# Kernel tuning notes

Measured on AMD Instinct MI355X. Metric: run time of the kernel, lower is better.

Reference implementation:

```python
import jax, jax.numpy as jnp
import numpy as np

N, C, T, V = 32, 64, 256, 25
IC, NS = 16, 3  # inter_channels = C // 4, num_subset = 3
EPS = 1e-5


def _bn(x, g, b, m, v):
    # inference-mode BatchNorm2d over channel dim of [N, C, T, V]
    scale = g / jnp.sqrt(v + EPS)
    return (x - m[:, None, None]) * scale[:, None, None] + b[:, None, None]


def _conv1x1(x, w, b):
    # 1x1 Conv2d on [N, C, T, V]; w: [O, C], b: [O]
    return jnp.einsum('nctv,oc->notv', x, w) + b[None, :, None, None]


def setup_inputs() -> dict:
    key = jax.random.key(0)
    ks = iter(jax.random.split(key, 40))
    def nrm(shape, s=0.05):
        return jax.random.normal(next(ks), shape, jnp.float32) * s
    inp = {}
    inp['feature'] = jax.random.normal(next(ks), (N, C, T, V), jnp.float32)
    inp['hidden'] = jax.random.normal(next(ks), (N, C, T, V), jnp.float32)
    inp['A'] = jax.random.uniform(next(ks), (NS, V, V), jnp.float32) * 0.1
    inp['PA'] = jnp.full((NS, V, V), 1e-6, jnp.float32)
    inp['conv_a_w'] = nrm((NS, IC, C)); inp['conv_a_b'] = nrm((NS, IC))
    inp['conv_b_w'] = nrm((NS, IC, C)); inp['conv_b_b'] = nrm((NS, IC))
    inp['conv_d_w'] = nrm((NS, C, C));  inp['conv_d_b'] = nrm((NS, C))
    inp['gbn_g'] = 0.5 + jax.random.uniform(next(ks), (C,), jnp.float32)
    inp['gbn_b'] = nrm((C,))
    inp['gbn_m'] = nrm((C,))
    inp['gbn_v'] = 0.5 + jax.random.uniform(next(ks), (C,), jnp.float32)
    inp['tcn_w'] = nrm((C, C, 9, 1)); inp['tcn_b'] = nrm((C,))
    inp['tbn_g'] = 0.5 + jax.random.uniform(next(ks), (C,), jnp.float32)
    inp['tbn_b'] = nrm((C,))
    inp['tbn_m'] = nrm((C,))
    inp['tbn_v'] = 0.5 + jax.random.uniform(next(ks), (C,), jnp.float32)
    for nme in ['W_ir', 'W_ii', 'W_in', 'W_hr', 'W_hi', 'W_hh']:
        inp[nme] = nrm((C, C))
    for nme in ['b_ir', 'b_ii', 'b_in']:
        inp[nme] = nrm((C,))
    return inp


def _tcn_gcn(h, A, PA, caw, cab, cbw, cbb, cdw, cdb,
             gbn_g, gbn_b, gbn_m, gbn_v, tcn_w, tcn_b,
             tbn_g, tbn_b, tbn_m, tbn_v):
    # unit_gcn (in == out -> down is identity)
    Aeff = A + PA  # [NS, V, V]
    scale = 1.0 / (IC * T)
    y = 0.0
    h_flat = h.reshape(N, C * T, V)
    for i in range(NS):
        a = _conv1x1(h, caw[i], cab[i])            # [N, IC, T, V]
        b = _conv1x1(h, cbw[i], cbb[i])            # [N, IC, T, V]
        A1 = a.transpose(0, 3, 1, 2).reshape(N, V, IC * T)
        A2 = b.reshape(N, IC * T, V)
        att = jax.nn.softmax(jnp.einsum('nvk,nkw->nvw', A1, A2) * scale, axis=-2)
        att = att + Aeff[i]                         # [N, V, V]
        z = jnp.einsum('nkv,nvw->nkw', h_flat, att).reshape(N, C, T, V)
        y = y + _conv1x1(z, cdw[i], cdb[i])
    gcn_out = jax.nn.relu(_bn(y, gbn_g, gbn_b, gbn_m, gbn_v) + h)
    # unit_tcn: (9,1) conv, pad (4,0), stride 1
    t = jax.lax.conv_general_dilated(
        gcn_out, tcn_w, window_strides=(1, 1), padding=[(4, 4), (0, 0)],
        dimension_numbers=('NCHW', 'OIHW', 'NCHW'))
    t = t + tcn_b[None, :, None, None]
    t = _bn(t, tbn_g, tbn_b, tbn_m, tbn_v)
    # residual is identity (in==out, stride 1)
    return jax.nn.relu(t + h)


def reference(feature, hidden, A, PA, conv_a_w, conv_a_b, conv_b_w, conv_b_b,
              conv_d_w, conv_d_b, gbn_g, gbn_b, gbn_m, gbn_v, tcn_w, tcn_b,
              tbn_g, tbn_b, tbn_m, tbn_v, W_ir, b_ir, W_ii, b_ii, W_in, b_in,
              W_hr, W_hi, W_hh):
    msg = _tcn_gcn(hidden, A, PA, conv_a_w, conv_a_b, conv_b_w, conv_b_b,
                   conv_d_w, conv_d_b, gbn_g, gbn_b, gbn_m, gbn_v,
                   tcn_w, tcn_b, tbn_g, tbn_b, tbn_m, tbn_v)
    feat = feature.transpose(0, 2, 3, 1).reshape(N, T * V, C)
    msg2 = msg.transpose(0, 2, 3, 1).reshape(N, T * V, C)
    hid2 = hidden.transpose(0, 2, 3, 1).reshape(N, T * V, C)
    r = jax.nn.sigmoid(feat @ W_ir.T + b_ir + msg2 @ W_hr.T)
    z = jax.nn.sigmoid(feat @ W_ii.T + b_ii + msg2 @ W_hi.T)
    n = jnp.tanh(feat @ W_in.T + b_in + r * (msg2 @ W_hh.T))
    h_new = (1.0 - z) * n + z * hid2
    return h_new.reshape(N, T, V, C).transpose(0, 3, 1, 2)
```

## Files before the change

### kernel.cpp

```cpp
#include <hip/hip_runtime.h>
#include <math.h>

#define TV 6400
#define NTOT 32

typedef __attribute__((ext_vector_type(8))) short short8;
typedef __attribute__((ext_vector_type(4))) short short4v;
typedef __attribute__((ext_vector_type(4))) float f32x4;

__device__ __forceinline__ float b2f(short s) {
  unsigned u = ((unsigned)(unsigned short)s) << 16;
  return __uint_as_float(u);
}
__device__ __forceinline__ short f2b(float f) {
  unsigned u = __float_as_uint(f);
  u = (u + 0x7FFF + ((u >> 16) & 1)) >> 16;
  return (short)u;
}

__global__ __launch_bounds__(256) void pack_kernel(
    const float* __restrict__ tcn_w, const float* __restrict__ caw,
    const float* __restrict__ cbw, const float* __restrict__ cdw,
    const float* __restrict__ W_ir, const float* __restrict__ W_ii,
    const float* __restrict__ W_in, const float* __restrict__ W_hr,
    const float* __restrict__ W_hi, const float* __restrict__ W_hh,
    const float* __restrict__ cab, const float* __restrict__ cbb,
    const float* __restrict__ b_ir, const float* __restrict__ b_ii,
    const float* __restrict__ b_in,
    short* __restrict__ P, float* __restrict__ Pb)
{
  int idx = blockIdx.x * 256 + threadIdx.x;
  if (idx < 9984) {
    int lane = idx & 63;
    int rest = idx >> 6;
    int c = rest & 1;
    rest >>= 1;
    int mloc = lane & 15, kb = c * 32 + (lane >> 4) * 8;
    short8 v;
    if (rest < 6) {
      int m = rest * 16 + mloc;
      for (int i = 0; i < 8; ++i)
        v[i] = f2b(m < 48 ? caw[m * 64 + kb + i] : cbw[(m - 48) * 64 + kb + i]);
    } else if (rest < 18) {
      int m = (rest - 6) * 16 + mloc;
      for (int i = 0; i < 8; ++i) v[i] = f2b(cdw[m * 64 + kb + i]);
    } else if (rest < 30) {
      int m = (rest - 18) * 16 + mloc;
      const float* W = (m < 64) ? W_ir : (m < 128 ? W_ii : W_in);
      int mr = m & 63;
      for (int i = 0; i < 8; ++i) v[i] = f2b(W[mr * 64 + kb + i]);
    } else if (rest < 42) {
      int m = (rest - 30) * 16 + mloc;
      const float* W = (m < 64) ? W_hr : (m < 128 ? W_hi : W_hh);
      int mr = m & 63;
      for (int i = 0; i < 8; ++i) v[i] = f2b(W[mr * 64 + kb + i]);
    } else {
      int t = rest - 42;
      int kk = t >> 2, mf = t & 3;
      int o = mf * 16 + mloc;
      for (int i = 0; i < 8; ++i) v[i] = f2b(tcn_w[o * 576 + (kb + i) * 9 + kk]);
    }
    *(short8*)(P + (size_t)idx * 8) = v;
  } else if (idx < 9984 + 288) {
    int r = idx - 9984;
    if (r < 96) Pb[r] = (r < 48) ? cab[r] : cbb[r - 48];
    else {
      int q = r - 96;
      Pb[r] = (q < 64) ? b_ir[q] : (q < 128 ? b_ii[q - 64] : b_in[q - 128]);
    }
  }
}

__global__ __launch_bounds__(256) void convert_kernel(
    const float* __restrict__ hid, const float* __restrict__ feat,
    short* __restrict__ hidK, short* __restrict__ featK)
{
  int j = blockIdx.x * 256 + threadIdx.x;
  int gy = blockIdx.y;
  int n = blockIdx.z;
  const float* src = ((gy < 8) ? hid : feat) + ((long)n * 64 + (long)(gy & 7) * 8) * TV + j;
  short* dst = ((gy < 8) ? hidK : featK) + (((long)n * 8 + (gy & 7)) * TV + j) * 8;
  short8 o;
#pragma unroll
  for (int i = 0; i < 8; ++i) o[i] = f2b(src[(long)i * TV]);
  *(short8*)dst = o;
}

__global__ __launch_bounds__(256) void ab_gemm(
    const short8* __restrict__ Wp, const short8* __restrict__ Bk,
    short* __restrict__ Cout, const float* __restrict__ bias)
{
  const int tid = threadIdx.x;
  const int lane = tid & 63, w = tid >> 6;
  const int q = lane >> 4, lj = lane & 15;
  const int j0 = blockIdx.x * 128;
  const int n = blockIdx.y;
  const short8* Bn = Bk + (long)n * 8 * TV;
  short* Cn = Cout + (long)n * 96 * TV;

  f32x4 acc[6][2];
  for (int a = 0; a < 6; ++a) for (int b = 0; b < 2; ++b)
    acc[a][b] = (f32x4){0.f, 0.f, 0.f, 0.f};

  for (int c = 0; c < 2; ++c) {
    short8 bf0 = Bn[(long)(c * 4 + q) * TV + j0 + (w * 2 + 0) * 16 + lj];
    short8 bf1 = Bn[(long)(c * 4 + q) * TV + j0 + (w * 2 + 1) * 16 + lj];
#pragma unroll
    for (int mf = 0; mf < 6; ++mf) {
      short8 af = Wp[(mf * 2 + c) * 64 + lane];
      acc[mf][0] = __builtin_amdgcn_mfma_f32_16x16x32_bf16(af, bf0, acc[mf][0], 0, 0, 0);
      acc[mf][1] = __builtin_amdgcn_mfma_f32_16x16x32_bf16(af, bf1, acc[mf][1], 0, 0, 0);
    }
  }
#pragma unroll
  for (int mf = 0; mf < 6; ++mf) {
    int k0 = mf * 16 + q * 4;
    int g = k0 >> 3, i0 = k0 & 7;
    float bv[4];
#pragma unroll
    for (int r = 0; r < 4; ++r) bv[r] = bias[k0 + r];
#pragma unroll
    for (int jf = 0; jf < 2; ++jf) {
      int j = j0 + (w * 2 + jf) * 16 + lj;
      short4v o4;
#pragma unroll
      for (int r = 0; r < 4; ++r) o4[r] = f2b(acc[mf][jf][r] + bv[r]);
      *(short4v*)(Cn + ((long)g * TV + j) * 8 + i0) = o4;
    }
  }
}

__global__ __launch_bounds__(256) void att_partial(
    const short* __restrict__ abK, float* __restrict__ partial)
{
  const int ch = blockIdx.x, i = blockIdx.y, n = blockIdx.z;
  __shared__ float sA[6400], sB[6400];
  const int tid = threadIdx.x;
  const long nb = (long)n * 96 * TV;
  const int t0 = ch * 16;
  for (int idx = tid; idx < 800; idx += 256) {
    int gh = idx / 400, jl = idx - gh * 400;
    long j = (long)t0 * 25 + jl;
    short8 va = *(const short8*)&abK[nb + ((long)(2 * i + gh) * TV + j) * 8];
    short8 vb = *(const short8*)&abK[nb + ((long)(6 + 2 * i + gh) * TV + j) * 8];
#pragma unroll
    for (int e = 0; e < 8; ++e) {
      sA[(gh * 8 + e) * 400 + jl] = b2f(va[e]);
      sB[(gh * 8 + e) * 400 + jl] = b2f(vb[e]);
    }
  }
  __syncthreads();
  const int a0 = tid >> 4, b0 = tid & 15;
  const int v1 = a0 + 16, w1 = b0 + 16;
  const int v1c = (v1 < 25) ? v1 : 0, w1c = (w1 < 25) ? w1 : 0;
  float acc00 = 0, acc01 = 0, acc10 = 0, acc11 = 0;
#pragma unroll 8
  for (int r = 0; r < 256; ++r) {
    float av0 = sA[r * 25 + a0], av1 = sA[r * 25 + v1c];
    float bw0 = sB[r * 25 + b0], bw1 = sB[r * 25 + w1c];
    acc00 += av0 * bw0; acc01 += av0 * bw1;
    acc10 += av1 * bw0; acc11 += av1 * bw1;
  }
  const float scale = 1.0f / 4096.0f;
  float* pp = partial + (((long)(n * 3 + i) * 16) + ch) * 625;
  pp[a0 * 25 + b0] = acc00 * scale;
  if (w1 < 25) pp[a0 * 25 + w1] = acc01 * scale;
  if (v1 < 25) pp[v1 * 25 + b0] = acc10 * scale;
  if (v1 < 25 && w1 < 25) pp[v1 * 25 + w1] = acc11 * scale;
}

__global__ __launch_bounds__(256) void att_reduce(
    const float* __restrict__ partial, const float* __restrict__ Amat,
    const float* __restrict__ PAmat, short* __restrict__ attP)
{
  const int i = blockIdx.x, n = blockIdx.y;
  __shared__ float sL[625];
  const int tid = threadIdx.x;
  const float* pp = partial + ((long)(n * 3 + i) * 16) * 625;
  for (int idx = tid; idx < 625; idx += 256) {
    float s = 0.f;
#pragma unroll
    for (int c = 0; c < 16; ++c) s += pp[c * 625 + idx];
    sL[idx] = s;
  }
  __syncthreads();
  if (tid < 25) {
    const int w = tid;
    float mx = -1e30f;
#pragma unroll
    for (int v = 0; v < 25; ++v) mx = fmaxf(mx, sL[v * 25 + w]);
    float e[25];
    float s = 0.f;
#pragma unroll
    for (int v = 0; v < 25; ++v) { e[v] = __expf(sL[v * 25 + w] - mx); s += e[v]; }
    float inv = 1.f / s;
#pragma unroll
    for (int v = 0; v < 25; ++v)
      sL[v * 25 + w] = e[v] * inv + Amat[i * 625 + v * 25 + w] + PAmat[i * 625 + v * 25 + w];
  }
  __syncthreads();
  if (tid < 128) {
    int wf = tid >> 6, lane = tid & 63;
    int q = lane >> 4, lj = lane & 15;
    int w = wf * 16 + lj;
    short8 o = {0, 0, 0, 0, 0, 0, 0, 0};
    if (w < 25) {
#pragma unroll
      for (int e2 = 0; e2 < 8; ++e2) {
        int v = q * 8 + e2;
        if (v < 25) o[e2] = f2b(sL[v * 25 + w]);
      }
    }
    *(short8*)(attP + (size_t)(((long)(n * 3 + i) * 2 + wf) * 64 + lane) * 8) = o;
  }
}

#define UST 114
#define OST 101
__global__ __launch_bounds__(256) void gcn_fused(
    const short8* __restrict__ Wu, const short8* __restrict__ attP,
    const short8* __restrict__ hidK, const float* __restrict__ cdb,
    const float* __restrict__ gg, const float* __restrict__ gb,
    const float* __restrict__ gm, const float* __restrict__ gv,
    short* __restrict__ gcnK)
{
  __shared__ short uT[192 * UST];
  __shared__ short sOut[64 * OST];
  __shared__ float A2[64], B2[64];
  const int tid = threadIdx.x;
  if (tid < 64) {
    float sc = gg[tid] * rsqrtf(gv[tid] + 1e-5f);
    A2[tid] = sc;
    float bias = cdb[tid] + cdb[64 + tid] + cdb[128 + tid];
    B2[tid] = bias * sc + (gb[tid] - gm[tid] * sc);
  }
  const int lane = tid & 63, w = tid >> 6;
  const int q = lane >> 4, lj = lane & 15;
  const int tt = blockIdx.x, n = blockIdx.y;
  const int jb = tt * 100;
  const short8* Hn = hidK + (long)n * 8 * TV;

  f32x4 uacc[3][7];
  for (int a = 0; a < 3; ++a) for (int b = 0; b < 7; ++b)
    uacc[a][b] = (f32x4){0.f, 0.f, 0.f, 0.f};
  for (int c = 0; c < 2; ++c) {
    short8 bf[7];
#pragma unroll
    for (int jf = 0; jf < 7; ++jf)
      bf[jf] = Hn[(long)(c * 4 + q) * TV + jb + jf * 16 + lj];
#pragma unroll
    for (int ml = 0; ml < 3; ++ml) {
      short8 af = Wu[((w * 3 + ml) * 2 + c) * 64 + lane];
#pragma unroll
      for (int jf = 0; jf < 7; ++jf)
        uacc[ml][jf] = __builtin_amdgcn_mfma_f32_16x16x32_bf16(af, bf[jf], uacc[ml][jf], 0, 0, 0);
    }
  }
#pragma unroll
  for (int ml = 0; ml < 3; ++ml) {
    int row0 = (w * 3 + ml) * 16 + q * 4;
#pragma unroll
    for (int jf = 0; jf < 7; ++jf) {
      int col = jf * 16 + lj;
#pragma unroll
      for (int r = 0; r < 4; ++r)
        uT[(row0 + r) * UST + col] = f2b(uacc[ml][jf][r]);
    }
  }
  __syncthreads();

  const int colt = w * 25;
  short8 attA[6];
#pragma unroll
  for (int i = 0; i < 3; ++i)
#pragma unroll
    for (int wf = 0; wf < 2; ++wf)
      attA[i * 2 + wf] = attP[((long)(n * 3 + i) * 2 + wf) * 64 + lane];

  f32x4 macc[2][4];
  for (int a = 0; a < 2; ++a) for (int b = 0; b < 4; ++b)
    macc[a][b] = (f32x4){0.f, 0.f, 0.f, 0.f};
#pragma unroll
  for (int i = 0; i < 3; ++i) {
#pragma unroll
    for (int of = 0; of < 4; ++of) {
      int row = i * 64 + of * 16 + lj;
      short8 bf;
#pragma unroll
      for (int e = 0; e < 8; ++e)
        bf[e] = uT[row * UST + colt + q * 8 + e];
      macc[0][of] = __builtin_amdgcn_mfma_f32_16x16x32_bf16(attA[i * 2 + 0], bf, macc[0][of], 0, 0, 0);
      macc[1][of] = __builtin_amdgcn_mfma_f32_16x16x32_bf16(attA[i * 2 + 1], bf, macc[1][of], 0, 0, 0);
    }
  }
#pragma unroll
  for (int wf = 0; wf < 2; ++wf)
#pragma unroll
    for (int of = 0; of < 4; ++of)
#pragma unroll
      for (int r = 0; r < 4; ++r) {
        int wl = wf * 16 + q * 4 + r;
        if (wl < 25)
          sOut[(of * 16 + lj) * OST + colt + wl] = f2b(macc[wf][of][r]);
      }
  __syncthreads();

  const short* HnS = (const short*)Hn;
  short* Gn = gcnK + (long)n * 64 * TV;
  for (int u2 = tid; u2 < 800; u2 += 256) {
    int col = u2 % 100, og = u2 / 100;
    long ubase = ((long)og * TV + jb + col) * 8;
    short8 h8 = *(const short8*)&HnS[ubase];
    short8 o8;
#pragma unroll
    for (int e = 0; e < 8; ++e) {
      int o = og * 8 + e;
      float acc = b2f(sOut[o * OST + col]);
      float vv = fmaxf(acc * A2[o] + B2[o] + b2f(h8[e]), 0.f);
      o8[e] = f2b(vv);
    }
    *(short8*)&Gn[ubase] = o8;
  }
}

__global__ __launch_bounds__(256) void tcn_mfma(
    const short8* __restrict__ wTp, const short8* __restrict__ gcnK,
    const short* __restrict__ hidK, const float* __restrict__ tcn_b,
    const float* __restrict__ pbg, const float* __restrict__ pbb,
    const float* __restrict__ pbm, const float* __restrict__ pbv,
    short* __restrict__ msgK)
{
  __shared__ float A2[64], B2[64];
  const int tid = threadIdx.x;
  if (tid < 64) {
    float sc = pbg[tid] * rsqrtf(pbv[tid] + 1e-5f);
    A2[tid] = sc;
    B2[tid] = tcn_b[tid] * sc + (pbb[tid] - pbm[tid] * sc);
  }
  __syncthreads();
  const int lane = tid & 63, w = tid >> 6;
  const int q = lane >> 4, lj = lane & 15;
  const int j0 = blockIdx.x * 128;
  const int n = blockIdx.y;
  const short8* Bn = gcnK + (long)n * 8 * TV;
  const short8 zero8 = {0, 0, 0, 0, 0, 0, 0, 0};

  f32x4 acc[4][2];
  for (int a = 0; a < 4; ++a) for (int b = 0; b < 2; ++b)
    acc[a][b] = (f32x4){0.f, 0.f, 0.f, 0.f};

  for (int kk = 0; kk < 9; ++kk) {
    const int shift = (kk - 4) * 25;
    for (int c = 0; c < 2; ++c) {
      short8 bfv[2];
#pragma unroll
      for (int jf = 0; jf < 2; ++jf) {
        int col = j0 + (w * 2 + jf) * 16 + lj + shift;
        bool valid = ((unsigned)col < (unsigned)TV);
        short8 t = Bn[(long)(c * 4 + q) * TV + (valid ? col : 0)];
        bfv[jf] = valid ? t : zero8;
      }
#pragma unroll
      for (int mf = 0; mf < 4; ++mf) {
        short8 af = wTp[((kk * 4 + mf) * 2 + c) * 64 + lane];
        acc[mf][0] = __builtin_amdgcn_mfma_f32_16x16x32_bf16(af, bfv[0], acc[mf][0], 0, 0, 0);
        acc[mf][1] = __builtin_amdgcn_mfma_f32_16x16x32_bf16(af, bfv[1], acc[mf][1], 0, 0, 0);
      }
    }
  }

  short* Mn = msgK + (long)n * 64 * TV;
  const short* Hn = hidK + (long)n * 64 * TV;
#pragma unroll
  for (int mf = 0; mf < 4; ++mf) {
    int k0 = mf * 16 + q * 4;
    int g = k0 >> 3, i0 = k0 & 7;
#pragma unroll
    for (int jf = 0; jf < 2; ++jf) {
      int j = j0 + (w * 2 + jf) * 16 + lj;
      long base = ((long)g * TV + j) * 8 + i0;
      short4v h4 = *(const short4v*)&Hn[base];
      short4v o4;
#pragma unroll
      for (int r = 0; r < 4; ++r) {
        float v = acc[mf][jf][r] * A2[k0 + r] + B2[k0 + r] + b2f(h4[r]);
        o4[r] = f2b(fmaxf(v, 0.f));
      }
      *(short4v*)&Mn[base] = o4;
    }
  }
}

__global__ __launch_bounds__(256) void gru_mfma(
    const short8* __restrict__ WFp, const short8* __restrict__ WHp,
    const float* __restrict__ bF, const short8* __restrict__ featK,
    const short8* __restrict__ msgK, const short* __restrict__ hidK,
    float* __restrict__ outp)
{
  __shared__ __align__(16) char smem[49152];
  __shared__ float sBias[192];
  short8* sW = (short8*)smem;
  float* sOut = (float*)smem;
  const int tid = threadIdx.x;
  for (int idx = tid; idx < 1536; idx += 256) {
    sW[idx] = WFp[idx];
    sW[1536 + idx] = WHp[idx];
  }
  if (tid < 192) sBias[tid] = bF[tid];
  __syncthreads();

  const int lane = tid & 63, w = tid >> 6;
  const int q = lane >> 4, lj = lane & 15;
  const int j0 = blockIdx.x * 64;
  const int n = blockIdx.y;
  const int j = j0 + w * 16 + lj;
  const short8* Fn = featK + (long)n * 8 * TV;
  const short8* Mn = msgK + (long)n * 8 * TV;

  f32x4 accF[12], accH[12];
  for (int a = 0; a < 12; ++a) {
    accF[a] = (f32x4){0.f, 0.f, 0.f, 0.f};
    accH[a] = (f32x4){0.f, 0.f, 0.f, 0.f};
  }
  for (int c = 0; c < 2; ++c) {
    short8 bFf = Fn[(long)(c * 4 + q) * TV + j];
    short8 bHf = Mn[(long)(c * 4 + q) * TV + j];
#pragma unroll
    for (int mf = 0; mf < 12; ++mf) {
      short8 af = sW[(mf * 2 + c) * 64 + lane];
      accF[mf] = __builtin_amdgcn_mfma_f32_16x16x32_bf16(af, bFf, accF[mf], 0, 0, 0);
      short8 ah = sW[1536 + (mf * 2 + c) * 64 + lane];
      accH[mf] = __builtin_amdgcn_mfma_f32_16x16x32_bf16(ah, bHf, accH[mf], 0, 0, 0);
    }
  }
  __syncthreads();

  const short* Hn = hidK + (long)n * 64 * TV;
#pragma unroll
  for (int mf = 0; mf < 4; ++mf) {
    int k0 = mf * 16 + q * 4;
    int g = k0 >> 3, i0 = k0 & 7;
    short4v h4 = *(const short4v*)&Hn[((long)g * TV + j) * 8 + i0];
#pragma unroll
    for (int r = 0; r < 4; ++r) {
      int o = k0 + r;
      float rp = accF[mf][r] + sBias[o] + accH[mf][r];
      float zp = accF[mf + 4][r] + sBias[64 + o] + accH[mf + 4][r];
      float np = accF[mf + 8][r] + sBias[128 + o];
      float rv = 1.f / (1.f + __expf(-rp));
      float zv = 1.f / (1.f + __expf(-zp));
      float nn = tanhf(np + rv * accH[mf + 8][r]);
      float hv = b2f(h4[r]);
      sOut[o * 68 + (w * 16 + lj)] = (1.f - zv) * nn + zv * hv;
    }
  }
  __syncthreads();
  float* On = outp + (long)n * 64 * TV;
  for (int u2 = tid; u2 < 1024; u2 += 256) {
    int row = u2 >> 4, c4 = u2 & 15;
    float4 vv = *(const float4*)&sOut[row * 68 + c4 * 4];
    *(float4*)&On[(long)row * TV + j0 + c4 * 4] = vv;
  }
}

extern "C" void kernel_launch(void* const* d_in, const int* in_sizes, int n_in,
                              void* d_out, int out_size, void* d_ws, size_t ws_size,
                              hipStream_t stream)
{
  const float* feature = (const float*)d_in[0];
  const float* hidden  = (const float*)d_in[1];
  const float* Amat    = (const float*)d_in[2];
  const float* PAmat   = (const float*)d_in[3];
  const float* caw = (const float*)d_in[4];
  const float* cab = (const float*)d_in[5];
  const float* cbw = (const float*)d_in[6];
  const float* cbb = (const float*)d_in[7];
  const float* cdw = (const float*)d_in[8];
  const float* cdb = (const float*)d_in[9];
  const float* gbn_g = (const float*)d_in[10];
  const float* gbn_b = (const float*)d_in[11];
  const float* gbn_m = (const float*)d_in[12];
  const float* gbn_v = (const float*)d_in[13];
  const float* tcn_w = (const float*)d_in[14];
  const float* tcn_b = (const float*)d_in[15];
  const float* tbn_g = (const float*)d_in[16];
  const float* tbn_b = (const float*)d_in[17];
  const float* tbn_m = (const float*)d_in[18];
  const float* tbn_v = (const float*)d_in[19];
  const float* W_ir = (const float*)d_in[20];
  const float* W_ii = (const float*)d_in[21];
  const float* W_in = (const float*)d_in[22];
  const float* W_hr = (const float*)d_in[23];
  const float* W_hi = (const float*)d_in[24];
  const float* W_hh = (const float*)d_in[25];
  const float* b_ir = (const float*)d_in[26];
  const float* b_ii = (const float*)d_in[27];
  const float* b_in = (const float*)d_in[28];
  float* out = (float*)d_out;

  int Nc = NTOT;
  while (Nc > 1) {
    size_t need = (size_t)352 * TV * 2 * Nc + (size_t)Nc * 30000 * 4 +
                  (size_t)Nc * 3072 * 2 + 79872 * 2 + 288 * 4 + 4096;
    if (need <= ws_size) break;
    Nc >>= 1;
  }

  char* p = (char*)d_ws;
  short* hidK = (short*)p;  p += (size_t)Nc * 64 * TV * 2;
  short* featK = (short*)p; p += (size_t)Nc * 64 * TV * 2;
  short* abK = (short*)p;   p += (size_t)Nc * 96 * TV * 2;
  short* gcnK = (short*)p;  p += (size_t)Nc * 64 * TV * 2;
  short* msgK = (short*)p;  p += (size_t)Nc * 64 * TV * 2;
  float* partial = (float*)p; p += (size_t)Nc * 30000 * 4;
  short* attP = (short*)p;    p += (size_t)Nc * 3072 * 2;
  p = (char*)(((size_t)p + 15) & ~(size_t)15);
  short* P = (short*)p;       p += 79872 * 2;
  float* Pb = (float*)p;

  pack_kernel<<<dim3(41), dim3(256), 0, stream>>>(
      tcn_w, caw, cbw, cdw, W_ir, W_ii, W_in, W_hr, W_hi, W_hh,
      cab, cbb, b_ir, b_ii, b_in, P, Pb);

  const long s64 = (long)64 * TV;
  for (int c0 = 0; c0 < NTOT; c0 += Nc) {
    const float* hidc = hidden + (long)c0 * s64;
    const float* featc = feature + (long)c0 * s64;
    float* outc = out + (long)c0 * s64;

    convert_kernel<<<dim3(25, 16, Nc), 256, 0, stream>>>(hidc, featc, hidK, featK);
    ab_gemm<<<dim3(50, Nc), 256, 0, stream>>>(
        (const short8*)P, (const short8*)hidK, abK, Pb);
    att_partial<<<dim3(16, 3, Nc), 256, 0, stream>>>(abK, partial);
    att_reduce<<<dim3(3, Nc), 256, 0, stream>>>(partial, Amat, PAmat, attP);
    gcn_fused<<<dim3(64, Nc), 256, 0, stream>>>(
        (const short8*)P + 768, (const short8*)attP, (const short8*)hidK,
        cdb, gbn_g, gbn_b, gbn_m, gbn_v, gcnK);
    tcn_mfma<<<dim3(50, Nc), 256, 0, stream>>>(
        (const short8*)P + 5376, (const short8*)gcnK, hidK, tcn_b,
        tbn_g, tbn_b, tbn_m, tbn_v, msgK);
    gru_mfma<<<dim3(100, Nc), 256, 0, stream>>>(
        (const short8*)P + 2304, (const short8*)P + 3840, Pb + 96,
        (const short8*)featK, (const short8*)msgK, hidK, outc);
  }
}
```

Before: 366.6 us.

## Vectorize GCN LDS reads, stage TCN weights in LDS, use fast GRU activations

The GCN kernel re-lays out the intermediate U tile so each 25-wide group is padded to 32 columns. This allows a single 16-byte LDS read per MFMA operand instead of eight scalar reads, and the output buffer now aliases the U buffer. The TCN kernel copies all 9-tap weights (about 72KB) into shared memory once per block instead of reading them from global memory in the inner loop, which may reduce occupancy. The GRU kernel swaps division and tanhf for rcp-based sigmoid and exp-based tanh, and writes output directly to global memory instead of staging it through LDS. This removes a barrier but makes each 16-lane group write 64 contiguous bytes per row.

```diff
diff --git a/kernel.cpp b/kernel.cpp
--- a/kernel.cpp
+++ b/kernel.cpp
@@ -16,6 +16,14 @@
   unsigned u = __float_as_uint(f);
   u = (u + 0x7FFF + ((u >> 16) & 1)) >> 16;
   return (short)u;
+}
+__device__ __forceinline__ float fsig(float x) {
+  return __builtin_amdgcn_rcpf(1.f + __expf(-x));
+}
+__device__ __forceinline__ float ftanh(float x) {
+  float x2 = fminf(fmaxf(2.f * x, -80.f), 80.f);
+  float t = __expf(x2);
+  return (t - 1.f) * __builtin_amdgcn_rcpf(t + 1.f);
 }
 
 __global__ __launch_bounds__(256) void pack_kernel(
@@ -215,7 +223,7 @@
   }
 }
 
-#define UST 114
+#define UST 136
 #define OST 101
 __global__ __launch_bounds__(256) void gcn_fused(
     const short8* __restrict__ Wu, const short8* __restrict__ attP,
@@ -224,9 +232,9 @@
     const float* __restrict__ gm, const float* __restrict__ gv,
     short* __restrict__ gcnK)
 {
-  __shared__ short uT[192 * UST];
-  __shared__ short sOut[64 * OST];
+  __shared__ __align__(16) short uT[192 * UST];
   __shared__ float A2[64], B2[64];
+  short* sOut = uT;
   const int tid = threadIdx.x;
   if (tid < 64) {
     float sc = gg[tid] * rsqrtf(gv[tid] + 1e-5f);
@@ -234,6 +242,11 @@
     float bias = cdb[tid] + cdb[64 + tid] + cdb[128 + tid];
     B2[tid] = bias * sc + (gb[tid] - gm[tid] * sc);
   }
+  for (int idx = tid; idx < 5376; idx += 256) {
+    int row = idx / 28, rr = idx - row * 28;
+    int g = rr / 7, s = 25 + (rr - g * 7);
+    uT[row * UST + g * 32 + s] = 0;
+  }
   const int lane = tid & 63, w = tid >> 6;
   const int q = lane >> 4, lj = lane & 15;
   const int tt = blockIdx.x, n = blockIdx.y;
@@ -262,9 +275,12 @@
 #pragma unroll
     for (int jf = 0; jf < 7; ++jf) {
       int col = jf * 16 + lj;
-#pragma unroll
-      for (int r = 0; r < 4; ++r)
-        uT[(row0 + r) * UST + col] = f2b(uacc[ml][jf][r]);
+      if (col < 100) {
+        int cc = (col / 25) * 32 + (col % 25);
+#pragma unroll
+        for (int r = 0; r < 4; ++r)
+          uT[(row0 + r) * UST + cc] = f2b(uacc[ml][jf][r]);
+      }
     }
   }
   __syncthreads();
@@ -285,14 +301,12 @@
 #pragma unroll
     for (int of = 0; of < 4; ++of) {
       int row = i * 64 + of * 16 + lj;
-      short8 bf;
-#pragma unroll
-      for (int e = 0; e < 8; ++e)
-        bf[e] = uT[row * UST + colt + q * 8 + e];
+      short8 bf = *(const short8*)&uT[row * UST + w * 32 + q * 8];
       macc[0][of] = __builtin_amdgcn_mfma_f32_16x16x32_bf16(attA[i * 2 + 0], bf, macc[0][of], 0, 0, 0);
       macc[1][of] = __builtin_amdgcn_mfma_f32_16x16x32_bf16(attA[i * 2 + 1], bf, macc[1][of], 0, 0, 0);
     }
   }
+  __syncthreads();
 #pragma unroll
   for (int wf = 0; wf < 2; ++wf)
 #pragma unroll
@@ -330,8 +344,10 @@
     const float* __restrict__ pbm, const float* __restrict__ pbv,
     short* __restrict__ msgK)
 {
+  __shared__ __align__(16) short8 sW[4608];
   __shared__ float A2[64], B2[64];
   const int tid = threadIdx.x;
+  for (int idx = tid; idx < 4608; idx += 256) sW[idx] = wTp[idx];
   if (tid < 64) {
     float sc = pbg[tid] * rsqrtf(pbv[tid] + 1e-5f);
     A2[tid] = sc;
@@ -362,7 +378,7 @@
       }
 #pragma unroll
       for (int mf = 0; mf < 4; ++mf) {
-        short8 af = wTp[((kk * 4 + mf) * 2 + c) * 64 + lane];
+        short8 af = sW[((kk * 4 + mf) * 2 + c) * 64 + lane];
         acc[mf][0] = __builtin_amdgcn_mfma_f32_16x16x32_bf16(af, bfv[0], acc[mf][0], 0, 0, 0);
         acc[mf][1] = __builtin_amdgcn_mfma_f32_16x16x32_bf16(af, bfv[1], acc[mf][1], 0, 0, 0);
       }
@@ -397,10 +413,8 @@
     const short8* __restrict__ msgK, const short* __restrict__ hidK,
     float* __restrict__ outp)
 {
-  __shared__ __align__(16) char smem[49152];
+  __shared__ __align__(16) short8 sW[3072];
   __shared__ float sBias[192];
-  short8* sW = (short8*)smem;
-  float* sOut = (float*)smem;
   const int tid = threadIdx.x;
   for (int idx = tid; idx < 1536; idx += 256) {
     sW[idx] = WFp[idx];
@@ -433,9 +447,9 @@
       accH[mf] = __builtin_amdgcn_mfma_f32_16x16x32_bf16(ah, bHf, accH[mf], 0, 0, 0);
     }
   }
-  __syncthreads();
 
   const short* Hn = hidK + (long)n * 64 * TV;
+  float* On = outp + (long)n * 64 * TV;
 #pragma unroll
   for (int mf = 0; mf < 4; ++mf) {
     int k0 = mf * 16 + q * 4;
@@ -447,19 +461,12 @@
       float rp = accF[mf][r] + sBias[o] + accH[mf][r];
       float zp = accF[mf + 4][r] + sBias[64 + o] + accH[mf + 4][r];
       float np = accF[mf + 8][r] + sBias[128 + o];
-      float rv = 1.f / (1.f + __expf(-rp));
-      float zv = 1.f / (1.f + __expf(-zp));
-      float nn = tanhf(np + rv * accH[mf + 8][r]);
+      float rv = fsig(rp);
+      float zv = fsig(zp);
+      float nn = ftanh(np + rv * accH[mf + 8][r]);
       float hv = b2f(h4[r]);
-      sOut[o * 68 + (w * 16 + lj)] = (1.f - zv) * nn + zv * hv;
-    }
-  }
-  __syncthreads();
-  float* On = outp + (long)n * 64 * TV;
-  for (int u2 = tid; u2 < 1024; u2 += 256) {
-    int row = u2 >> 4, c4 = u2 & 15;
-    float4 vv = *(const float4*)&sOut[row * 68 + c4 * 4];
-    *(float4*)&On[(long)row * TV + j0 + c4 * 4] = vv;
+      On[(long)o * TV + j] = (1.f - zv) * nn + zv * hv;
+    }
   }
 }
 
```

After: 367.0 us. About the same (+0.1%).
